# Kernel optimization log

Measured on AMD Instinct MI355X. Metric: run time of the kernel, lower is better.

Reference implementation:

```python
import jax, jax.numpy as jnp
import numpy as np

B, T_IN, T_OUT = 512, 256, 128
V, N, EH, DH, SD = 256, 1024, 64, 128, 32


def _lstm_scan(gx_seq, W_hh, h0, c0):
    """gx_seq: (T, B, 4H) precomputed input-side gates (incl. bias).
    PyTorch LSTMCell gate order: i, f, g, o."""
    def step(carry, gx):
        h, c = carry
        g = gx + h @ W_hh.T                       # (B, 4H)
        i, f, gg, o = jnp.split(g, 4, axis=-1)
        c2 = jax.nn.sigmoid(f) * c + jax.nn.sigmoid(i) * jnp.tanh(gg)
        h2 = jax.nn.sigmoid(o) * jnp.tanh(c2)
        return (h2, c2), h2
    (hT, cT), hs = jax.lax.scan(step, (h0, c0), gx_seq)
    return hT, hs


def _forward(inp_onehot, zia, tgt, fortza,
             enc_Wih, enc_Whh, enc_b, sg_W, sg_b,
             Wc_W, Wc_b, dec_Wih, dec_Whh, dec_b, out_W, out_b):
    Bb = inp_onehot.shape[0]
    dt = inp_onehot.dtype
    # ---- encoder: input projection hoisted out of the recurrence ----
    # enc_in = concat([x_t, zia]); zia is constant over t, so its gate
    # contribution is computed once (same math as the per-step cat+GEMM).
    Wx, Wz = enc_Wih[:, :V], enc_Wih[:, V:]          # (4EH,V), (4EH,N)
    gx_const = zia @ Wz.T + enc_b                    # (B, 4EH)
    gx_enc = jnp.einsum('btv,gv->tbg', inp_onehot, Wx) + gx_const[None]
    h0 = jnp.zeros((Bb, EH), dt)
    h_enc, _ = _lstm_scan(gx_enc, enc_Whh, h0, h0)   # (B, EH)
    # ---- soul update ----
    sg = jnp.concatenate([h_enc, fortza], axis=-1) @ sg_W.T + sg_b
    gate = jax.nn.sigmoid(sg[:, :SD])
    update = jnp.tanh(sg[:, SD:])
    fortza_new = gate * fortza + (1.0 - gate) * update
    # ---- decoder init ----
    dh0 = jnp.tanh(jnp.concatenate([h_enc, zia], axis=-1) @ Wc_W.T + Wc_b)
    dc0 = jnp.zeros_like(dh0)
    # ---- decoder recurrence ----
    gx_dec = jnp.einsum('btv,gv->tbg', tgt, dec_Wih) + dec_b
    _, dhs = _lstm_scan(gx_dec, dec_Whh, dh0, dc0)   # (T_out, B, DH)
    # ---- output projection: split cat([dh, fortza_new]) @ W.T ----
    Wd, Wf = out_W[:, :DH], out_W[:, DH:]
    logits = (jnp.einsum('tbh,vh->btv', dhs, Wd)
              + (fortza_new @ Wf.T)[:, None, :] + out_b)
    return logits, fortza_new


def setup_inputs() -> dict:
    key = jax.random.key(0)
    ks = jax.random.split(key, 20)
    f32 = jnp.float32
    def nrm(k, shape, s=0.05):
        return jax.random.normal(k, shape, f32) * s
    inp_idx = jax.random.randint(ks[0], (B, T_IN), 0, V)
    tgt_idx = jax.random.randint(ks[1], (B, T_OUT), 0, V)
    return {
        'inp_onehot': jax.nn.one_hot(inp_idx, V, dtype=f32),
        'zia': jax.random.uniform(ks[2], (B, N), f32),
        'tgt': jax.nn.one_hot(tgt_idx, V, dtype=f32),
        'fortza': nrm(ks[3], (B, SD), 0.5),
        'enc_Wih': nrm(ks[4], (4 * EH, V + N)),
        'enc_Whh': nrm(ks[5], (4 * EH, EH)),
        'enc_b': nrm(ks[6], (4 * EH,)),
        'sg_W': nrm(ks[7], (2 * SD, EH + SD)),
        'sg_b': nrm(ks[8], (2 * SD,)),
        'Wc_W': nrm(ks[9], (DH, EH + N)),
        'Wc_b': nrm(ks[10], (DH,)),
        'dec_Wih': nrm(ks[11], (4 * DH, V)),
        'dec_Whh': nrm(ks[12], (4 * DH, DH)),
        'dec_b': nrm(ks[13], (4 * DH,)),
        'out_W': nrm(ks[14], (V, DH + SD)),
        'out_b': nrm(ks[15], (V,)),
    }


def reference(inp_onehot, zia, tgt, fortza,
              enc_Wih, enc_Whh, enc_b, sg_W, sg_b,
              Wc_W, Wc_b, dec_Wih, dec_Whh, dec_b, out_W, out_b):
    return _forward(inp_onehot, zia, tgt, fortza,
                    enc_Wih, enc_Whh, enc_b, sg_W, sg_b,
                    Wc_W, Wc_b, dec_Wih, dec_Whh, dec_b, out_W, out_b)
```

## Files before the change

### kernel.cpp

```cpp
#include <hip/hip_runtime.h>
#include <hip/hip_bf16.h>

#define BATCH 512
#define TIN   256
#define TOUT  128
#define VOC   256
#define NZ    1024
#define EHID  64
#define DHID  128
#define SDIM  32

typedef __attribute__((ext_vector_type(8))) short bf16x8;
typedef __attribute__((ext_vector_type(4))) float f32x4;

__device__ __forceinline__ float bf2f(unsigned short u) {
  return __uint_as_float(((unsigned)u) << 16);
}
__device__ __forceinline__ unsigned short f2bf(float f) {
  unsigned u = __float_as_uint(f);
  u = u + 0x7FFFu + ((u >> 16) & 1u);
  return (unsigned short)(u >> 16);
}
__device__ __forceinline__ float sigf(float x) { return 1.0f / (1.0f + __expf(-x)); }
__device__ __forceinline__ float tanh_(float x) { return 1.0f - 2.0f / (1.0f + __expf(2.0f * x)); }

__device__ __forceinline__ void sync_lds() {
  asm volatile("s_waitcnt lgkmcnt(0)\n\ts_barrier" ::: "memory");
}

__device__ __forceinline__ bf16x8 pack8(float4 a, float4 b) {
  bf16x8 r;
  r[0] = (short)f2bf(a.x); r[1] = (short)f2bf(a.y);
  r[2] = (short)f2bf(a.z); r[3] = (short)f2bf(a.w);
  r[4] = (short)f2bf(b.x); r[5] = (short)f2bf(b.y);
  r[6] = (short)f2bf(b.z); r[7] = (short)f2bf(b.w);
  return r;
}

__device__ __forceinline__ void dev_findidx(const float* __restrict__ src,
                                            int pos, int lane,
                                            int* __restrict__ out) {
  float4 v = ((const float4*)src)[(size_t)pos * 64 + lane];
  int comp = v.x > 0.5f ? 0 : (v.y > 0.5f ? 1 : (v.z > 0.5f ? 2 : 3));
  bool hit = (v.x > 0.5f) || (v.y > 0.5f) || (v.z > 0.5f) || (v.w > 0.5f);
  int cand = hit ? lane * 4 + comp : (1 << 30);
#pragma unroll
  for (int off = 32; off > 0; off >>= 1) {
    int o = __shfl_xor(cand, off);
    cand = cand < o ? cand : o;
  }
  if (lane == 0) out[pos] = cand < VOC ? cand : VOC - 1;
}

__global__ __launch_bounds__(256) void k_pre(
    const float* __restrict__ enc_Wih, const float* __restrict__ enc_b,
    const float* __restrict__ inp_onehot, const float* __restrict__ zia,
    float* __restrict__ WxT, float* __restrict__ gxc, int* __restrict__ enc_idx) {
  int blk = blockIdx.x, tid = threadIdx.x;
  if (blk < 64) {
    __shared__ float T[32][36];
    int r = tid >> 3, c = (tid & 7) * 4;
    int g0 = (blk >> 3) * 32, v0 = (blk & 7) * 32;
    float4 v = *(const float4*)(enc_Wih + (size_t)(g0 + r) * (VOC + NZ) + v0 + c);
    float bias = enc_b[g0 + r];
    T[c + 0][r] = v.x + bias; T[c + 1][r] = v.y + bias;
    T[c + 2][r] = v.z + bias; T[c + 3][r] = v.w + bias;
    __syncthreads();
    *(float4*)(WxT + (size_t)(v0 + r) * 256 + g0 + c) = *(const float4*)&T[r][c];
  } else if (blk < 192) {
    __shared__ float As[32][36], Bs[32][36];
    int q = blk - 64;
    int b0 = (q & 15) * 32, g0 = (q >> 4) * 32;
    int ldr = tid >> 3, ldc = (tid & 7) * 4;
    int tx = tid & 15, ty = tid >> 4;
    float a00 = 0.f, a01 = 0.f, a10 = 0.f, a11 = 0.f;
    for (int kc = 0; kc < NZ; kc += 32) {
      float4 av = *(const float4*)(zia + (size_t)(b0 + ldr) * NZ + kc + ldc);
      float4 bv = *(const float4*)(enc_Wih + (size_t)(g0 + ldr) * (VOC + NZ) + VOC + kc + ldc);
      __syncthreads();
      As[ldc + 0][ldr] = av.x; As[ldc + 1][ldr] = av.y;
      As[ldc + 2][ldr] = av.z; As[ldc + 3][ldr] = av.w;
      Bs[ldc + 0][ldr] = bv.x; Bs[ldc + 1][ldr] = bv.y;
      Bs[ldc + 2][ldr] = bv.z; Bs[ldc + 3][ldr] = bv.w;
      __syncthreads();
#pragma unroll
      for (int k = 0; k < 32; ++k) {
        float x0 = As[k][tx * 2], x1 = As[k][tx * 2 + 1];
        float y0 = Bs[k][ty * 2], y1 = Bs[k][ty * 2 + 1];
        a00 += x0 * y0; a01 += x0 * y1; a10 += x1 * y0; a11 += x1 * y1;
      }
    }
    float* o = gxc + (size_t)(b0 + tx * 2) * 256 + g0 + ty * 2;
    o[0] = a00; o[1] = a01; o[256] = a10; o[257] = a11;
  } else {
    int widx = (blk - 192) * 4 + (tid >> 6);
    int lane = tid & 63;
#pragma unroll 2
    for (int i = 0; i < 16; ++i)
      dev_findidx(inp_onehot, widx * 16 + i, lane, enc_idx);
  }
}

#define ESTR 72
__global__ __launch_bounds__(256) void k_enc_fused(
    const float* __restrict__ enc_Whh, const float* __restrict__ WxT,
    const float* __restrict__ gxc, const int* __restrict__ enc_idx,
    float* __restrict__ h_enc,
    const float* __restrict__ dec_Wih, const float* __restrict__ dec_b,
    const float* __restrict__ out_W, const float* __restrict__ tgt,
    float* __restrict__ WdecT, float* __restrict__ WdT, int* __restrict__ dec_idx) {
  int blk = blockIdx.x, tid = threadIdx.x;
  if (blk < 128) {
    __shared__ unsigned short hA[2][16 * ESTR];
    __shared__ int idx_s[4][TIN];
    int b0 = blk * 4;
    int w = tid >> 6, lane = tid & 63, n = lane & 15, quad = lane >> 4;
    int j = w * 16 + n;

    bf16x8 Bf[4][2];
#pragma unroll
    for (int ty = 0; ty < 4; ++ty)
#pragma unroll
      for (int kb = 0; kb < 2; ++kb) {
        const float* s = enc_Whh + (size_t)(ty * 64 + j) * EHID + kb * 32 + quad * 8;
        Bf[ty][kb] = pack8(*(const float4*)s, *(const float4*)(s + 4));
      }
    for (int i = tid; i < 16 * ESTR; i += 256) { hA[0][i] = 0; hA[1][i] = 0; }
    for (int i = tid; i < 4 * TIN; i += 256)
      idx_s[i >> 8][i & 255] = enc_idx[(size_t)(b0 + (i >> 8)) * TIN + (i & 255)];
    float gc[4];
#pragma unroll
    for (int ty = 0; ty < 4; ++ty) gc[ty] = gxc[(size_t)(b0 + quad) * 256 + ty * 64 + j];
    __syncthreads();

    float gx[4];
    {
      int id0 = idx_s[quad][0];
#pragma unroll
      for (int ty = 0; ty < 4; ++ty) gx[ty] = WxT[(size_t)id0 * 256 + ty * 64 + j];
    }
    float c0 = 0.0f, h = 0.0f;
    for (int t = 0; t < TIN; ++t) {
      const unsigned short* cur = hA[t & 1];
      bf16x8 a[2];
#pragma unroll
      for (int kb = 0; kb < 2; ++kb)
        a[kb] = *(const bf16x8*)(cur + n * ESTR + kb * 32 + quad * 8);
      float gxn[4];
      int tn = (t + 1 < TIN) ? t + 1 : t;
      int idn = idx_s[quad][tn];
#pragma unroll
      for (int ty = 0; ty < 4; ++ty) gxn[ty] = WxT[(size_t)idn * 256 + ty * 64 + j];
      f32x4 acc[4];
#pragma unroll
      for (int ty = 0; ty < 4; ++ty) {
        f32x4 z; z[0] = gx[ty] + gc[ty]; z[1] = 0.f; z[2] = 0.f; z[3] = 0.f;
        z = __builtin_amdgcn_mfma_f32_16x16x32_bf16(a[0], Bf[ty][0], z, 0, 0, 0);
        z = __builtin_amdgcn_mfma_f32_16x16x32_bf16(a[1], Bf[ty][1], z, 0, 0, 0);
        acc[ty] = z;
      }
      float gi = acc[0][0], gf = acc[1][0], gg = acc[2][0], go = acc[3][0];
      c0 = sigf(gf) * c0 + sigf(gi) * tanh_(gg);
      h = sigf(go) * tanh_(c0);
      hA[(t + 1) & 1][(quad * 4) * ESTR + j] = f2bf(h);
      gx[0] = gxn[0]; gx[1] = gxn[1]; gx[2] = gxn[2]; gx[3] = gxn[3];
      sync_lds();
    }
    h_enc[(size_t)(b0 + quad) * EHID + j] = h;
  } else if (blk < 256) {
    __shared__ float T[32][36];
    int q = blk - 128;
    int r = tid >> 3, c = (tid & 7) * 4;
    int g0 = (q >> 3) * 32, v0 = (q & 7) * 32;
    float4 v = *(const float4*)(dec_Wih + (size_t)(g0 + r) * VOC + v0 + c);
    float bias = dec_b[g0 + r];
    T[c + 0][r] = v.x + bias; T[c + 1][r] = v.y + bias;
    T[c + 2][r] = v.z + bias; T[c + 3][r] = v.w + bias;
    __syncthreads();
    *(float4*)(WdecT + (size_t)(v0 + r) * 512 + g0 + c) = *(const float4*)&T[r][c];
  } else if (blk < 288) {
    __shared__ float T2[32][36];
    int q = blk - 256;
    int r = tid >> 3, c = (tid & 7) * 4;
    int v0 = (q >> 2) * 32, k0 = (q & 3) * 32;
    float4 v = *(const float4*)(out_W + (size_t)(v0 + r) * (DHID + SDIM) + k0 + c);
    T2[c + 0][r] = v.x; T2[c + 1][r] = v.y; T2[c + 2][r] = v.z; T2[c + 3][r] = v.w;
    __syncthreads();
    *(float4*)(WdT + (size_t)(k0 + r) * 256 + v0 + c) = *(const float4*)&T2[r][c];
  } else {
    int widx = (blk - 288) * 4 + (tid >> 6);
    int lane = tid & 63;
#pragma unroll 2
    for (int i = 0; i < 16; ++i)
      dev_findidx(tgt, widx * 16 + i, lane, dec_idx);
  }
}

__global__ __launch_bounds__(256) void k_mid(
    const float* __restrict__ h_enc, const float* __restrict__ fortza,
    const float* __restrict__ sg_W, const float* __restrict__ sg_b,
    const float* __restrict__ out_W, const float* __restrict__ out_b,
    const float* __restrict__ zia, const float* __restrict__ Wc_W,
    const float* __restrict__ Wc_b,
    float* __restrict__ out_fortza, float* __restrict__ fout,
    float* __restrict__ dh0) {
  int blk = blockIdx.x, tid = threadIdx.x;
  if (blk < 512) {
    __shared__ float hf[EHID], fz[SDIM], sg_s[2 * SDIM], fn[SDIM];
    int b = blk;
    if (tid < EHID) hf[tid] = h_enc[b * EHID + tid];
    if (tid >= EHID && tid < EHID + SDIM)
      fz[tid - EHID] = fortza[(size_t)b * SDIM + (tid - EHID)];
    __syncthreads();
    if (tid < 2 * SDIM) {
      float acc = sg_b[tid];
      const float* row = sg_W + (size_t)tid * (EHID + SDIM);
      for (int k = 0; k < EHID; ++k) acc += hf[k] * row[k];
      for (int jj = 0; jj < SDIM; ++jj) acc += fz[jj] * row[EHID + jj];
      sg_s[tid] = acc;
    }
    __syncthreads();
    if (tid < SDIM) {
      float gate = sigf(sg_s[tid]);
      float upd = tanh_(sg_s[SDIM + tid]);
      float v = gate * fz[tid] + (1.0f - gate) * upd;
      fn[tid] = v;
      out_fortza[(size_t)b * SDIM + tid] = v;
    }
    __syncthreads();
    {
      float acc = out_b[tid];
      const float* row = out_W + (size_t)tid * (DHID + SDIM) + DHID;
      for (int jj = 0; jj < SDIM; ++jj) acc += fn[jj] * row[jj];
      fout[b * VOC + tid] = acc;
    }
  } else {
    __shared__ float As[32][36], Bs[32][36];
    int q = blk - 512;
    int b0 = (q & 15) * 32, v0 = (q >> 4) * 32;
    int ldr = tid >> 3, ldc = (tid & 7) * 4;
    int tx = tid & 15, ty = tid >> 4;
    float a00 = 0.f, a01 = 0.f, a10 = 0.f, a11 = 0.f;
    for (int kc = 0; kc < EHID + NZ; kc += 32) {
      float4 av;
      if (kc < EHID)
        av = *(const float4*)(h_enc + (size_t)(b0 + ldr) * EHID + kc + ldc);
      else
        av = *(const float4*)(zia + (size_t)(b0 + ldr) * NZ + (kc - EHID) + ldc);
      float4 bv = *(const float4*)(Wc_W + (size_t)(v0 + ldr) * (EHID + NZ) + kc + ldc);
      __syncthreads();
      As[ldc + 0][ldr] = av.x; As[ldc + 1][ldr] = av.y;
      As[ldc + 2][ldr] = av.z; As[ldc + 3][ldr] = av.w;
      Bs[ldc + 0][ldr] = bv.x; Bs[ldc + 1][ldr] = bv.y;
      Bs[ldc + 2][ldr] = bv.z; Bs[ldc + 3][ldr] = bv.w;
      __syncthreads();
#pragma unroll
      for (int k = 0; k < 32; ++k) {
        float x0 = As[k][tx * 2], x1 = As[k][tx * 2 + 1];
        float y0 = Bs[k][ty * 2], y1 = Bs[k][ty * 2 + 1];
        a00 += x0 * y0; a01 += x0 * y1; a10 += x1 * y0; a11 += x1 * y1;
      }
    }
    float bb0 = Wc_b[v0 + ty * 2], bb1 = Wc_b[v0 + ty * 2 + 1];
    float* o = dh0 + (size_t)(b0 + tx * 2) * DHID + v0 + ty * 2;
    o[0] = tanh_(a00 + bb0); o[1] = tanh_(a01 + bb1);
    o[DHID] = tanh_(a10 + bb0); o[DHID + 1] = tanh_(a11 + bb1);
  }
}

#define DSTR 136
__global__ __launch_bounds__(512) void k_dec_logits(
    const float* __restrict__ dec_Whh, const float* __restrict__ WdecT,
    const int* __restrict__ dec_idx, const float* __restrict__ dh0,
    const float* __restrict__ WdT, const float* __restrict__ fout,
    float* __restrict__ out) {
  __shared__ unsigned short hA[2][16 * DSTR];
  __shared__ int idx_s[4][TOUT];
  int b0 = blockIdx.x * 4;
  int tid = threadIdx.x;
  int w = tid >> 6, lane = tid & 63, n = lane & 15, quad = lane >> 4;
  int j0 = w * 16, j = j0 + n;

  bf16x8 Bf[4][4];
#pragma unroll
  for (int ty = 0; ty < 4; ++ty)
#pragma unroll
    for (int kb = 0; kb < 4; ++kb) {
      const float* src = dec_Whh + (size_t)(ty * 128 + j0 + n) * DHID + kb * 32 + quad * 8;
      Bf[ty][kb] = pack8(*(const float4*)src, *(const float4*)(src + 4));
    }
  bf16x8 BfL[2][4];
  float fo[2];
  float* op[2];
#pragma unroll
  for (int p = 0; p < 2; ++p) {
    int v = (w * 2 + p) * 16 + n;
#pragma unroll
    for (int kb = 0; kb < 4; ++kb) {
      const float* src = WdT + (size_t)(kb * 32 + quad * 8) * 256 + v;
      bf16x8 r;
#pragma unroll
      for (int i = 0; i < 8; ++i) r[i] = (short)f2bf(src[i * 256]);
      BfL[p][kb] = r;
    }
    fo[p] = fout[(size_t)(b0 + quad) * VOC + v];
    op[p] = out + (size_t)(b0 + quad) * TOUT * VOC + v;
  }
  for (int i = tid; i < 16 * DSTR; i += 512) {
    int m = i / DSTR, k = i - m * DSTR;
    float v = (k < DHID && (m & 3) == 0) ? dh0[(size_t)(b0 + (m >> 2)) * DHID + k] : 0.0f;
    hA[0][i] = f2bf(v);
    hA[1][i] = 0;
  }
  for (int i = tid; i < 4 * TOUT; i += 512)
    idx_s[i >> 7][i & 127] = dec_idx[(size_t)(b0 + (i >> 7)) * TOUT + (i & 127)];
  __syncthreads();

  float gx[4];
  {
    int id0 = idx_s[quad][0];
#pragma unroll
    for (int ty = 0; ty < 4; ++ty) gx[ty] = WdecT[(size_t)id0 * 512 + ty * 128 + j];
  }
  float c0 = 0.0f;
  for (int t = 0; t < TOUT; ++t) {
    const unsigned short* cur = hA[t & 1];
    bf16x8 a[4];
#pragma unroll
    for (int kb = 0; kb < 4; ++kb)
      a[kb] = *(const bf16x8*)(cur + n * DSTR + kb * 32 + quad * 8);
    float gxn[4];
    int tn = (t + 1 < TOUT) ? t + 1 : t;
    int idn = idx_s[quad][tn];
#pragma unroll
    for (int ty = 0; ty < 4; ++ty) gxn[ty] = WdecT[(size_t)idn * 512 + ty * 128 + j];
    f32x4 acc[4];
#pragma unroll
    for (int ty = 0; ty < 4; ++ty) {
      f32x4 z; z[0] = gx[ty]; z[1] = 0.f; z[2] = 0.f; z[3] = 0.f;
#pragma unroll
      for (int kb = 0; kb < 4; ++kb)
        z = __builtin_amdgcn_mfma_f32_16x16x32_bf16(a[kb], Bf[ty][kb], z, 0, 0, 0);
      acc[ty] = z;
    }
    float gi = acc[0][0], gf = acc[1][0], gg = acc[2][0], go = acc[3][0];
    c0 = sigf(gf) * c0 + sigf(gi) * tanh_(gg);
    float h = sigf(go) * tanh_(c0);
    hA[(t + 1) & 1][(quad * 4) * DSTR + j] = f2bf(h);
    if (t > 0) {
#pragma unroll
      for (int p = 0; p < 2; ++p) {
        f32x4 z; z[0] = fo[p]; z[1] = 0.f; z[2] = 0.f; z[3] = 0.f;
#pragma unroll
        for (int kb = 0; kb < 4; ++kb)
          z = __builtin_amdgcn_mfma_f32_16x16x32_bf16(a[kb], BfL[p][kb], z, 0, 0, 0);
        *op[p] = z[0];
        op[p] += VOC;
      }
    }
    gx[0] = gxn[0]; gx[1] = gxn[1]; gx[2] = gxn[2]; gx[3] = gxn[3];
    sync_lds();
  }
  {
    const unsigned short* cur = hA[0];
    bf16x8 a[4];
#pragma unroll
    for (int kb = 0; kb < 4; ++kb)
      a[kb] = *(const bf16x8*)(cur + n * DSTR + kb * 32 + quad * 8);
#pragma unroll
    for (int p = 0; p < 2; ++p) {
      f32x4 z; z[0] = fo[p]; z[1] = 0.f; z[2] = 0.f; z[3] = 0.f;
#pragma unroll
      for (int kb = 0; kb < 4; ++kb)
        z = __builtin_amdgcn_mfma_f32_16x16x32_bf16(a[kb], BfL[p][kb], z, 0, 0, 0);
      *op[p] = z[0];
    }
  }
}

extern "C" void kernel_launch(void* const* d_in, const int* in_sizes, int n_in,
                              void* d_out, int out_size, void* d_ws, size_t ws_size,
                              hipStream_t stream) {
  const float* inp_onehot = (const float*)d_in[0];
  const float* zia     = (const float*)d_in[1];
  const float* tgt     = (const float*)d_in[2];
  const float* fortza  = (const float*)d_in[3];
  const float* enc_Wih = (const float*)d_in[4];
  const float* enc_Whh = (const float*)d_in[5];
  const float* enc_b   = (const float*)d_in[6];
  const float* sg_W    = (const float*)d_in[7];
  const float* sg_b    = (const float*)d_in[8];
  const float* Wc_W    = (const float*)d_in[9];
  const float* Wc_b    = (const float*)d_in[10];
  const float* dec_Wih = (const float*)d_in[11];
  const float* dec_Whh = (const float*)d_in[12];
  const float* dec_b   = (const float*)d_in[13];
  const float* out_W   = (const float*)d_in[14];
  const float* out_b   = (const float*)d_in[15];
  float* out = (float*)d_out;

  float* ws = (float*)d_ws;
  int* enc_idx  = (int*)d_ws;
  int* dec_idx  = enc_idx + BATCH * TIN;
  float* WxT    = ws + 196608;
  float* WdecT  = ws + 262144;
  float* WdT    = ws + 393216;
  float* gxc    = ws + 425984;
  float* h_enc  = ws + 557056;
  float* dh0    = ws + 589824;
  float* fout   = ws + 655360;

  k_pre<<<192 + 2048, 256, 0, stream>>>(
      enc_Wih, enc_b, inp_onehot, zia, WxT, gxc, enc_idx);
  k_enc_fused<<<288 + 1024, 256, 0, stream>>>(
      enc_Whh, WxT, gxc, enc_idx, h_enc,
      dec_Wih, dec_b, out_W, tgt, WdecT, WdT, dec_idx);
  k_mid<<<576, 256, 0, stream>>>(h_enc, fortza, sg_W, sg_b, out_W, out_b,
                                 zia, Wc_W, Wc_b,
                                 out + (size_t)BATCH * TOUT * VOC, fout, dh0);
  k_dec_logits<<<BATCH / 4, 512, 0, stream>>>(dec_Whh, WdecT, dec_idx, dh0,
                                              WdT, fout, out);
}
```

Before: 534.9 us.

## Fuse encoder, mid-stage and decoder into one per-batch-tile mega kernel

Reduces four launches to two. Weight transposes and the zia gate GEMM move into a table kernel, and a single 512-thread kernel per 4-row batch tile now does index finding, the encoder scan, the soul/decoder-init projections and the decoder-with-logits scan. Intermediates (indices, h_enc, dh0, fout) stay in LDS instead of going through global memory. The cost is that the encoder scan runs on only 4 of 8 waves while the others idle at barriers. The per-block Wc GEMM is also now done with scalar loops over 1088 elements instead of a tiled GEMM, which may lengthen the serial middle phase.

```diff
diff --git a/kernel.cpp b/kernel.cpp
--- a/kernel.cpp
+++ b/kernel.cpp
@@ -37,10 +37,9 @@
   return r;
 }
 
-__device__ __forceinline__ void dev_findidx(const float* __restrict__ src,
-                                            int pos, int lane,
-                                            int* __restrict__ out) {
-  float4 v = ((const float4*)src)[(size_t)pos * 64 + lane];
+__device__ __forceinline__ int dev_findidx(const float* __restrict__ src,
+                                           size_t row, int lane) {
+  float4 v = ((const float4*)src)[row * 64 + lane];
   int comp = v.x > 0.5f ? 0 : (v.y > 0.5f ? 1 : (v.z > 0.5f ? 2 : 3));
   bool hit = (v.x > 0.5f) || (v.y > 0.5f) || (v.z > 0.5f) || (v.w > 0.5f);
   int cand = hit ? lane * 4 + comp : (1 << 30);
@@ -49,13 +48,15 @@
     int o = __shfl_xor(cand, off);
     cand = cand < o ? cand : o;
   }
-  if (lane == 0) out[pos] = cand < VOC ? cand : VOC - 1;
-}
-
-__global__ __launch_bounds__(256) void k_pre(
+  return cand < VOC ? cand : VOC - 1;
+}
+
+__global__ __launch_bounds__(256) void k_tables(
     const float* __restrict__ enc_Wih, const float* __restrict__ enc_b,
-    const float* __restrict__ inp_onehot, const float* __restrict__ zia,
-    float* __restrict__ WxT, float* __restrict__ gxc, int* __restrict__ enc_idx) {
+    const float* __restrict__ dec_Wih, const float* __restrict__ dec_b,
+    const float* __restrict__ out_W, const float* __restrict__ zia,
+    float* __restrict__ WxT, float* __restrict__ WdecT, float* __restrict__ WdT,
+    float* __restrict__ gxc) {
   int blk = blockIdx.x, tid = threadIdx.x;
   if (blk < 64) {
     __shared__ float T[32][36];
@@ -68,8 +69,28 @@
     __syncthreads();
     *(float4*)(WxT + (size_t)(v0 + r) * 256 + g0 + c) = *(const float4*)&T[r][c];
   } else if (blk < 192) {
+    __shared__ float T[32][36];
+    int q = blk - 64;
+    int r = tid >> 3, c = (tid & 7) * 4;
+    int g0 = (q >> 3) * 32, v0 = (q & 7) * 32;
+    float4 v = *(const float4*)(dec_Wih + (size_t)(g0 + r) * VOC + v0 + c);
+    float bias = dec_b[g0 + r];
+    T[c + 0][r] = v.x + bias; T[c + 1][r] = v.y + bias;
+    T[c + 2][r] = v.z + bias; T[c + 3][r] = v.w + bias;
+    __syncthreads();
+    *(float4*)(WdecT + (size_t)(v0 + r) * 512 + g0 + c) = *(const float4*)&T[r][c];
+  } else if (blk < 224) {
+    __shared__ float T[32][36];
+    int q = blk - 192;
+    int r = tid >> 3, c = (tid & 7) * 4;
+    int v0 = (q >> 2) * 32, k0 = (q & 3) * 32;
+    float4 v = *(const float4*)(out_W + (size_t)(v0 + r) * (DHID + SDIM) + k0 + c);
+    T[c + 0][r] = v.x; T[c + 1][r] = v.y; T[c + 2][r] = v.z; T[c + 3][r] = v.w;
+    __syncthreads();
+    *(float4*)(WdT + (size_t)(k0 + r) * 256 + v0 + c) = *(const float4*)&T[r][c];
+  } else {
     __shared__ float As[32][36], Bs[32][36];
-    int q = blk - 64;
+    int q = blk - 224;
     int b0 = (q & 15) * 32, g0 = (q >> 4) * 32;
     int ldr = tid >> 3, ldc = (tid & 7) * 4;
     int tx = tid & 15, ty = tid >> 4;
@@ -92,31 +113,56 @@
     }
     float* o = gxc + (size_t)(b0 + tx * 2) * 256 + g0 + ty * 2;
     o[0] = a00; o[1] = a01; o[256] = a10; o[257] = a11;
-  } else {
-    int widx = (blk - 192) * 4 + (tid >> 6);
-    int lane = tid & 63;
+  }
+}
+
+#define ESTR 72
+#define DSTR 136
+__global__ __launch_bounds__(512) void k_mega(
+    const float* __restrict__ inp_onehot, const float* __restrict__ tgt,
+    const float* __restrict__ zia, const float* __restrict__ fortza,
+    const float* __restrict__ enc_Whh, const float* __restrict__ WxT,
+    const float* __restrict__ gxc,
+    const float* __restrict__ sg_W, const float* __restrict__ sg_b,
+    const float* __restrict__ out_W, const float* __restrict__ out_b,
+    const float* __restrict__ Wc_W, const float* __restrict__ Wc_b,
+    const float* __restrict__ dec_Whh, const float* __restrict__ WdecT,
+    const float* __restrict__ WdT,
+    float* __restrict__ out, float* __restrict__ out_fortza) {
+  __shared__ unsigned short hAe[2][16 * ESTR];
+  __shared__ unsigned short hAd[2][16 * DSTR];
+  __shared__ int   idx_e[4][TIN];
+  __shared__ int   idx_d[4][TOUT];
+  __shared__ float xs[4][EHID + NZ];
+  __shared__ float fouts[4][VOC];
+  __shared__ float dh0s[4][DHID];
+  __shared__ float fzs[4][SDIM], fns[4][SDIM];
+  __shared__ float sgs[4][2 * SDIM];
+
+  int b0 = blockIdx.x * 4;
+  int tid = threadIdx.x;
+  int w = tid >> 6, lane = tid & 63, n = lane & 15, quad = lane >> 4;
+
+  for (int i = tid; i < 2 * 16 * ESTR; i += 512) ((unsigned short*)hAe)[i] = 0;
 #pragma unroll 2
-    for (int i = 0; i < 16; ++i)
-      dev_findidx(inp_onehot, widx * 16 + i, lane, enc_idx);
-  }
-}
-
-#define ESTR 72
-__global__ __launch_bounds__(256) void k_enc_fused(
-    const float* __restrict__ enc_Whh, const float* __restrict__ WxT,
-    const float* __restrict__ gxc, const int* __restrict__ enc_idx,
-    float* __restrict__ h_enc,
-    const float* __restrict__ dec_Wih, const float* __restrict__ dec_b,
-    const float* __restrict__ out_W, const float* __restrict__ tgt,
-    float* __restrict__ WdecT, float* __restrict__ WdT, int* __restrict__ dec_idx) {
-  int blk = blockIdx.x, tid = threadIdx.x;
-  if (blk < 128) {
-    __shared__ unsigned short hA[2][16 * ESTR];
-    __shared__ int idx_s[4][TIN];
-    int b0 = blk * 4;
-    int w = tid >> 6, lane = tid & 63, n = lane & 15, quad = lane >> 4;
+  for (int it = 0; it < 128; ++it) {
+    int p = w * 128 + it;
+    int b = p >> 8, t = p & 255;
+    int idx = dev_findidx(inp_onehot, (size_t)(b0 + b) * TIN + t, lane);
+    if (lane == 0) idx_e[b][t] = idx;
+  }
+#pragma unroll 2
+  for (int it = 0; it < 64; ++it) {
+    int p = w * 64 + it;
+    int b = p >> 7, t = p & 127;
+    int idx = dev_findidx(tgt, (size_t)(b0 + b) * TOUT + t, lane);
+    if (lane == 0) idx_d[b][t] = idx;
+  }
+  __syncthreads();
+
+  if (w < 4) {
     int j = w * 16 + n;
-
+    int arow = n & 12;
     bf16x8 Bf[4][2];
 #pragma unroll
     for (int ty = 0; ty < 4; ++ty)
@@ -125,30 +171,25 @@
         const float* s = enc_Whh + (size_t)(ty * 64 + j) * EHID + kb * 32 + quad * 8;
         Bf[ty][kb] = pack8(*(const float4*)s, *(const float4*)(s + 4));
       }
-    for (int i = tid; i < 16 * ESTR; i += 256) { hA[0][i] = 0; hA[1][i] = 0; }
-    for (int i = tid; i < 4 * TIN; i += 256)
-      idx_s[i >> 8][i & 255] = enc_idx[(size_t)(b0 + (i >> 8)) * TIN + (i & 255)];
     float gc[4];
 #pragma unroll
     for (int ty = 0; ty < 4; ++ty) gc[ty] = gxc[(size_t)(b0 + quad) * 256 + ty * 64 + j];
-    __syncthreads();
-
     float gx[4];
     {
-      int id0 = idx_s[quad][0];
+      int id0 = idx_e[quad][0];
 #pragma unroll
       for (int ty = 0; ty < 4; ++ty) gx[ty] = WxT[(size_t)id0 * 256 + ty * 64 + j];
     }
     float c0 = 0.0f, h = 0.0f;
     for (int t = 0; t < TIN; ++t) {
-      const unsigned short* cur = hA[t & 1];
+      const unsigned short* cur = hAe[t & 1];
       bf16x8 a[2];
 #pragma unroll
       for (int kb = 0; kb < 2; ++kb)
-        a[kb] = *(const bf16x8*)(cur + n * ESTR + kb * 32 + quad * 8);
+        a[kb] = *(const bf16x8*)(cur + arow * ESTR + kb * 32 + quad * 8);
       float gxn[4];
       int tn = (t + 1 < TIN) ? t + 1 : t;
-      int idn = idx_s[quad][tn];
+      int idn = idx_e[quad][tn];
 #pragma unroll
       for (int ty = 0; ty < 4; ++ty) gxn[ty] = WxT[(size_t)idn * 256 + ty * 64 + j];
       f32x4 acc[4];
@@ -162,211 +203,152 @@
       float gi = acc[0][0], gf = acc[1][0], gg = acc[2][0], go = acc[3][0];
       c0 = sigf(gf) * c0 + sigf(gi) * tanh_(gg);
       h = sigf(go) * tanh_(c0);
-      hA[(t + 1) & 1][(quad * 4) * ESTR + j] = f2bf(h);
+      hAe[(t + 1) & 1][(quad * 4) * ESTR + j] = f2bf(h);
       gx[0] = gxn[0]; gx[1] = gxn[1]; gx[2] = gxn[2]; gx[3] = gxn[3];
       sync_lds();
     }
-    h_enc[(size_t)(b0 + quad) * EHID + j] = h;
-  } else if (blk < 256) {
-    __shared__ float T[32][36];
-    int q = blk - 128;
-    int r = tid >> 3, c = (tid & 7) * 4;
-    int g0 = (q >> 3) * 32, v0 = (q & 7) * 32;
-    float4 v = *(const float4*)(dec_Wih + (size_t)(g0 + r) * VOC + v0 + c);
-    float bias = dec_b[g0 + r];
-    T[c + 0][r] = v.x + bias; T[c + 1][r] = v.y + bias;
-    T[c + 2][r] = v.z + bias; T[c + 3][r] = v.w + bias;
-    __syncthreads();
-    *(float4*)(WdecT + (size_t)(v0 + r) * 512 + g0 + c) = *(const float4*)&T[r][c];
-  } else if (blk < 288) {
-    __shared__ float T2[32][36];
-    int q = blk - 256;
-    int r = tid >> 3, c = (tid & 7) * 4;
-    int v0 = (q >> 2) * 32, k0 = (q & 3) * 32;
-    float4 v = *(const float4*)(out_W + (size_t)(v0 + r) * (DHID + SDIM) + k0 + c);
-    T2[c + 0][r] = v.x; T2[c + 1][r] = v.y; T2[c + 2][r] = v.z; T2[c + 3][r] = v.w;
-    __syncthreads();
-    *(float4*)(WdT + (size_t)(k0 + r) * 256 + v0 + c) = *(const float4*)&T2[r][c];
+    xs[quad][j] = h;
   } else {
-    int widx = (blk - 288) * 4 + (tid >> 6);
-    int lane = tid & 63;
-#pragma unroll 2
-    for (int i = 0; i < 16; ++i)
-      dev_findidx(tgt, widx * 16 + i, lane, dec_idx);
-  }
-}
-
-__global__ __launch_bounds__(256) void k_mid(
-    const float* __restrict__ h_enc, const float* __restrict__ fortza,
-    const float* __restrict__ sg_W, const float* __restrict__ sg_b,
-    const float* __restrict__ out_W, const float* __restrict__ out_b,
-    const float* __restrict__ zia, const float* __restrict__ Wc_W,
-    const float* __restrict__ Wc_b,
-    float* __restrict__ out_fortza, float* __restrict__ fout,
-    float* __restrict__ dh0) {
-  int blk = blockIdx.x, tid = threadIdx.x;
-  if (blk < 512) {
-    __shared__ float hf[EHID], fz[SDIM], sg_s[2 * SDIM], fn[SDIM];
-    int b = blk;
-    if (tid < EHID) hf[tid] = h_enc[b * EHID + tid];
-    if (tid >= EHID && tid < EHID + SDIM)
-      fz[tid - EHID] = fortza[(size_t)b * SDIM + (tid - EHID)];
-    __syncthreads();
-    if (tid < 2 * SDIM) {
-      float acc = sg_b[tid];
-      const float* row = sg_W + (size_t)tid * (EHID + SDIM);
-      for (int k = 0; k < EHID; ++k) acc += hf[k] * row[k];
-      for (int jj = 0; jj < SDIM; ++jj) acc += fz[jj] * row[EHID + jj];
-      sg_s[tid] = acc;
-    }
-    __syncthreads();
-    if (tid < SDIM) {
-      float gate = sigf(sg_s[tid]);
-      float upd = tanh_(sg_s[SDIM + tid]);
-      float v = gate * fz[tid] + (1.0f - gate) * upd;
-      fn[tid] = v;
-      out_fortza[(size_t)b * SDIM + tid] = v;
-    }
-    __syncthreads();
-    {
-      float acc = out_b[tid];
-      const float* row = out_W + (size_t)tid * (DHID + SDIM) + DHID;
-      for (int jj = 0; jj < SDIM; ++jj) acc += fn[jj] * row[jj];
-      fout[b * VOC + tid] = acc;
-    }
-  } else {
-    __shared__ float As[32][36], Bs[32][36];
-    int q = blk - 512;
-    int b0 = (q & 15) * 32, v0 = (q >> 4) * 32;
-    int ldr = tid >> 3, ldc = (tid & 7) * 4;
-    int tx = tid & 15, ty = tid >> 4;
-    float a00 = 0.f, a01 = 0.f, a10 = 0.f, a11 = 0.f;
-    for (int kc = 0; kc < EHID + NZ; kc += 32) {
-      float4 av;
-      if (kc < EHID)
-        av = *(const float4*)(h_enc + (size_t)(b0 + ldr) * EHID + kc + ldc);
-      else
-        av = *(const float4*)(zia + (size_t)(b0 + ldr) * NZ + (kc - EHID) + ldc);
-      float4 bv = *(const float4*)(Wc_W + (size_t)(v0 + ldr) * (EHID + NZ) + kc + ldc);
-      __syncthreads();
-      As[ldc + 0][ldr] = av.x; As[ldc + 1][ldr] = av.y;
-      As[ldc + 2][ldr] = av.z; As[ldc + 3][ldr] = av.w;
-      Bs[ldc + 0][ldr] = bv.x; Bs[ldc + 1][ldr] = bv.y;
-      Bs[ldc + 2][ldr] = bv.z; Bs[ldc + 3][ldr] = bv.w;
-      __syncthreads();
-#pragma unroll
-      for (int k = 0; k < 32; ++k) {
-        float x0 = As[k][tx * 2], x1 = As[k][tx * 2 + 1];
-        float y0 = Bs[k][ty * 2], y1 = Bs[k][ty * 2 + 1];
-        a00 += x0 * y0; a01 += x0 * y1; a10 += x1 * y0; a11 += x1 * y1;
-      }
-    }
-    float bb0 = Wc_b[v0 + ty * 2], bb1 = Wc_b[v0 + ty * 2 + 1];
-    float* o = dh0 + (size_t)(b0 + tx * 2) * DHID + v0 + ty * 2;
-    o[0] = tanh_(a00 + bb0); o[1] = tanh_(a01 + bb1);
-    o[DHID] = tanh_(a10 + bb0); o[DHID + 1] = tanh_(a11 + bb1);
-  }
-}
-
-#define DSTR 136
-__global__ __launch_bounds__(512) void k_dec_logits(
-    const float* __restrict__ dec_Whh, const float* __restrict__ WdecT,
-    const int* __restrict__ dec_idx, const float* __restrict__ dh0,
-    const float* __restrict__ WdT, const float* __restrict__ fout,
-    float* __restrict__ out) {
-  __shared__ unsigned short hA[2][16 * DSTR];
-  __shared__ int idx_s[4][TOUT];
-  int b0 = blockIdx.x * 4;
-  int tid = threadIdx.x;
-  int w = tid >> 6, lane = tid & 63, n = lane & 15, quad = lane >> 4;
-  int j0 = w * 16, j = j0 + n;
-
-  bf16x8 Bf[4][4];
-#pragma unroll
-  for (int ty = 0; ty < 4; ++ty)
-#pragma unroll
-    for (int kb = 0; kb < 4; ++kb) {
-      const float* src = dec_Whh + (size_t)(ty * 128 + j0 + n) * DHID + kb * 32 + quad * 8;
-      Bf[ty][kb] = pack8(*(const float4*)src, *(const float4*)(src + 4));
-    }
-  bf16x8 BfL[2][4];
-  float fo[2];
-  float* op[2];
-#pragma unroll
-  for (int p = 0; p < 2; ++p) {
-    int v = (w * 2 + p) * 16 + n;
-#pragma unroll
-    for (int kb = 0; kb < 4; ++kb) {
-      const float* src = WdT + (size_t)(kb * 32 + quad * 8) * 256 + v;
-      bf16x8 r;
-#pragma unroll
-      for (int i = 0; i < 8; ++i) r[i] = (short)f2bf(src[i * 256]);
-      BfL[p][kb] = r;
-    }
-    fo[p] = fout[(size_t)(b0 + quad) * VOC + v];
-    op[p] = out + (size_t)(b0 + quad) * TOUT * VOC + v;
+    for (int t = 0; t < TIN; ++t) sync_lds();
+  }
+  __syncthreads();
+
+  for (int i = tid; i < 1024; i += 512) {
+    int b = i >> 8, q4 = i & 255;
+    float4 v = ((const float4*)(zia + (size_t)(b0 + b) * NZ))[q4];
+    *(float4*)&xs[b][EHID + q4 * 4] = v;
+  }
+  if (tid < 128) {
+    int b = tid >> 5, s = tid & 31;
+    fzs[b][s] = fortza[(size_t)(b0 + b) * SDIM + s];
+  }
+  __syncthreads();
+  if (tid < 256) {
+    int b = tid >> 6, o = tid & 63;
+    float acc = sg_b[o];
+    const float* row = sg_W + (size_t)o * (EHID + SDIM);
+#pragma unroll 8
+    for (int k = 0; k < EHID; ++k) acc += xs[b][k] * row[k];
+#pragma unroll
+    for (int k = 0; k < SDIM; ++k) acc += fzs[b][k] * row[EHID + k];
+    sgs[b][o] = acc;
+  }
+  {
+    int b = tid >> 7, v = tid & 127;
+    float acc = Wc_b[v];
+    const float4* wr = (const float4*)(Wc_W + (size_t)v * (EHID + NZ));
+    const float4* x4 = (const float4*)xs[b];
+#pragma unroll 8
+    for (int k4 = 0; k4 < (EHID + NZ) / 4; ++k4) {
+      float4 wv = wr[k4], xv = x4[k4];
+      acc += wv.x * xv.x + wv.y * xv.y + wv.z * xv.z + wv.w * xv.w;
+    }
+    dh0s[b][v] = tanh_(acc);
+  }
+  __syncthreads();
+  if (tid < 128) {
+    int b = tid >> 5, s = tid & 31;
+    float gate = sigf(sgs[b][s]);
+    float upd = tanh_(sgs[b][SDIM + s]);
+    float v = gate * fzs[b][s] + (1.0f - gate) * upd;
+    fns[b][s] = v;
+    out_fortza[(size_t)(b0 + b) * SDIM + s] = v;
+  }
+  __syncthreads();
+  for (int i = tid; i < 4 * VOC; i += 512) {
+    int b = i >> 8, v = i & 255;
+    float acc = out_b[v];
+    const float* row = out_W + (size_t)v * (DHID + SDIM) + DHID;
+#pragma unroll
+    for (int k = 0; k < SDIM; ++k) acc += fns[b][k] * row[k];
+    fouts[b][v] = acc;
   }
   for (int i = tid; i < 16 * DSTR; i += 512) {
     int m = i / DSTR, k = i - m * DSTR;
-    float v = (k < DHID && (m & 3) == 0) ? dh0[(size_t)(b0 + (m >> 2)) * DHID + k] : 0.0f;
-    hA[0][i] = f2bf(v);
-    hA[1][i] = 0;
-  }
-  for (int i = tid; i < 4 * TOUT; i += 512)
-    idx_s[i >> 7][i & 127] = dec_idx[(size_t)(b0 + (i >> 7)) * TOUT + (i & 127)];
-  __syncthreads();
-
-  float gx[4];
+    float v = (k < DHID && (m & 3) == 0) ? dh0s[m >> 2][k] : 0.0f;
+    hAd[0][i] = f2bf(v);
+    hAd[1][i] = 0;
+  }
+  __syncthreads();
+
   {
-    int id0 = idx_s[quad][0];
-#pragma unroll
-    for (int ty = 0; ty < 4; ++ty) gx[ty] = WdecT[(size_t)id0 * 512 + ty * 128 + j];
-  }
-  float c0 = 0.0f;
-  for (int t = 0; t < TOUT; ++t) {
-    const unsigned short* cur = hA[t & 1];
+    int j0 = w * 16, j = j0 + n;
+    int arow = n & 12;
+    bf16x8 Bf[4][4];
+#pragma unroll
+    for (int ty = 0; ty < 4; ++ty)
+#pragma unroll
+      for (int kb = 0; kb < 4; ++kb) {
+        const float* src = dec_Whh + (size_t)(ty * 128 + j) * DHID + kb * 32 + quad * 8;
+        Bf[ty][kb] = pack8(*(const float4*)src, *(const float4*)(src + 4));
+      }
+    bf16x8 BfL[2][4];
+    float fo[2];
+    float* op[2];
+#pragma unroll
+    for (int p = 0; p < 2; ++p) {
+      int v = (w * 2 + p) * 16 + n;
+#pragma unroll
+      for (int kb = 0; kb < 4; ++kb) {
+        const float* src = WdT + (size_t)(kb * 32 + quad * 8) * 256 + v;
+        bf16x8 r;
+#pragma unroll
+        for (int i = 0; i < 8; ++i) r[i] = (short)f2bf(src[i * 256]);
+        BfL[p][kb] = r;
+      }
+      fo[p] = fouts[quad][v];
+      op[p] = out + (size_t)(b0 + quad) * TOUT * VOC + v;
+    }
+    float gx[4];
+    {
+      int id0 = idx_d[quad][0];
+#pragma unroll
+      for (int ty = 0; ty < 4; ++ty) gx[ty] = WdecT[(size_t)id0 * 512 + ty * 128 + j];
+    }
+    float c0 = 0.0f;
+    for (int t = 0; t < TOUT; ++t) {
+      const unsigned short* cur = hAd[t & 1];
+      bf16x8 a[4];
+#pragma unroll
+      for (int kb = 0; kb < 4; ++kb)
+        a[kb] = *(const bf16x8*)(cur + arow * DSTR + kb * 32 + quad * 8);
+      float gxn[4];
+      int tn = (t + 1 < TOUT) ? t + 1 : t;
+      int idn = idx_d[quad][tn];
+#pragma unroll
+      for (int ty = 0; ty < 4; ++ty) gxn[ty] = WdecT[(size_t)idn * 512 + ty * 128 + j];
+      f32x4 acc[4];
+#pragma unroll
+      for (int ty = 0; ty < 4; ++ty) {
+        f32x4 z; z[0] = gx[ty]; z[1] = 0.f; z[2] = 0.f; z[3] = 0.f;
+#pragma unroll
+        for (int kb = 0; kb < 4; ++kb)
+          z = __builtin_amdgcn_mfma_f32_16x16x32_bf16(a[kb], Bf[ty][kb], z, 0, 0, 0);
+        acc[ty] = z;
+      }
+      float gi = acc[0][0], gf = acc[1][0], gg = acc[2][0], go = acc[3][0];
+      c0 = sigf(gf) * c0 + sigf(gi) * tanh_(gg);
+      float h = sigf(go) * tanh_(c0);
+      hAd[(t + 1) & 1][(quad * 4) * DSTR + j] = f2bf(h);
+      if (t > 0) {
+#pragma unroll
+        for (int p = 0; p < 2; ++p) {
+          f32x4 z; z[0] = fo[p]; z[1] = 0.f; z[2] = 0.f; z[3] = 0.f;
+#pragma unroll
+          for (int kb = 0; kb < 4; ++kb)
+            z = __builtin_amdgcn_mfma_f32_16x16x32_bf16(a[kb], BfL[p][kb], z, 0, 0, 0);
+          *op[p] = z[0];
+          op[p] += VOC;
+        }
+      }
+      gx[0] = gxn[0]; gx[1] = gxn[1]; gx[2] = gxn[2]; gx[3] = gxn[3];
+      sync_lds();
+    }
+    const unsigned short* cur = hAd[0];
     bf16x8 a[4];
 #pragma unroll
     for (int kb = 0; kb < 4; ++kb)
-      a[kb] = *(const bf16x8*)(cur + n * DSTR + kb * 32 + quad * 8);
-    float gxn[4];
-    int tn = (t + 1 < TOUT) ? t + 1 : t;
-    int idn = idx_s[quad][tn];
-#pragma unroll
-    for (int ty = 0; ty < 4; ++ty) gxn[ty] = WdecT[(size_t)idn * 512 + ty * 128 + j];
-    f32x4 acc[4];
-#pragma unroll
-    for (int ty = 0; ty < 4; ++ty) {
-      f32x4 z; z[0] = gx[ty]; z[1] = 0.f; z[2] = 0.f; z[3] = 0.f;
-#pragma unroll
-      for (int kb = 0; kb < 4; ++kb)
-        z = __builtin_amdgcn_mfma_f32_16x16x32_bf16(a[kb], Bf[ty][kb], z, 0, 0, 0);
-      acc[ty] = z;
-    }
-    float gi = acc[0][0], gf = acc[1][0], gg = acc[2][0], go = acc[3][0];
-    c0 = sigf(gf) * c0 + sigf(gi) * tanh_(gg);
-    float h = sigf(go) * tanh_(c0);
-    hA[(t + 1) & 1][(quad * 4) * DSTR + j] = f2bf(h);
-    if (t > 0) {
-#pragma unroll
-      for (int p = 0; p < 2; ++p) {
-        f32x4 z; z[0] = fo[p]; z[1] = 0.f; z[2] = 0.f; z[3] = 0.f;
-#pragma unroll
-        for (int kb = 0; kb < 4; ++kb)
-          z = __builtin_amdgcn_mfma_f32_16x16x32_bf16(a[kb], BfL[p][kb], z, 0, 0, 0);
-        *op[p] = z[0];
-        op[p] += VOC;
-      }
-    }
-    gx[0] = gxn[0]; gx[1] = gxn[1]; gx[2] = gxn[2]; gx[3] = gxn[3];
-    sync_lds();
-  }
-  {
-    const unsigned short* cur = hA[0];
-    bf16x8 a[4];
-#pragma unroll
-    for (int kb = 0; kb < 4; ++kb)
-      a[kb] = *(const bf16x8*)(cur + n * DSTR + kb * 32 + quad * 8);
+      a[kb] = *(const bf16x8*)(cur + arow * DSTR + kb * 32 + quad * 8);
 #pragma unroll
     for (int p = 0; p < 2; ++p) {
       f32x4 z; z[0] = fo[p]; z[1] = 0.f; z[2] = 0.f; z[3] = 0.f;
@@ -386,8 +368,8 @@
   const float* tgt     = (const float*)d_in[2];
   const float* fortza  = (const float*)d_in[3];
   const float* enc_Wih = (const float*)d_in[4];
+  const float* enc_b   = (const float*)d_in[6];
   const float* enc_Whh = (const float*)d_in[5];
-  const float* enc_b   = (const float*)d_in[6];
   const float* sg_W    = (const float*)d_in[7];
   const float* sg_b    = (const float*)d_in[8];
   const float* Wc_W    = (const float*)d_in[9];
@@ -400,24 +382,15 @@
   float* out = (float*)d_out;
 
   float* ws = (float*)d_ws;
-  int* enc_idx  = (int*)d_ws;
-  int* dec_idx  = enc_idx + BATCH * TIN;
-  float* WxT    = ws + 196608;
-  float* WdecT  = ws + 262144;
-  float* WdT    = ws + 393216;
-  float* gxc    = ws + 425984;
-  float* h_enc  = ws + 557056;
-  float* dh0    = ws + 589824;
-  float* fout   = ws + 655360;
-
-  k_pre<<<192 + 2048, 256, 0, stream>>>(
-      enc_Wih, enc_b, inp_onehot, zia, WxT, gxc, enc_idx);
-  k_enc_fused<<<288 + 1024, 256, 0, stream>>>(
-      enc_Whh, WxT, gxc, enc_idx, h_enc,
-      dec_Wih, dec_b, out_W, tgt, WdecT, WdT, dec_idx);
-  k_mid<<<576, 256, 0, stream>>>(h_enc, fortza, sg_W, sg_b, out_W, out_b,
-                                 zia, Wc_W, Wc_b,
-                                 out + (size_t)BATCH * TOUT * VOC, fout, dh0);
-  k_dec_logits<<<BATCH / 4, 512, 0, stream>>>(dec_Whh, WdecT, dec_idx, dh0,
-                                              WdT, fout, out);
-}
+  float* WxT    = ws;
+  float* WdecT  = ws + 65536;
+  float* WdT    = ws + 196608;
+  float* gxc    = ws + 229376;
+
+  k_tables<<<352, 256, 0, stream>>>(enc_Wih, enc_b, dec_Wih, dec_b, out_W, zia,
+                                    WxT, WdecT, WdT, gxc);
+  k_mega<<<BATCH / 4, 512, 0, stream>>>(
+      inp_onehot, tgt, zia, fortza, enc_Whh, WxT, gxc,
+      sg_W, sg_b, out_W, out_b, Wc_W, Wc_b, dec_Whh, WdecT, WdT,
+      out, out + (size_t)BATCH * TOUT * VOC);
+}
```

After: 673.3 us. 25.9% more time.
